# Performance work log

Measured on AMD Instinct MI355X. Metric: run time of the kernel, lower is better.

## Reference

```python
import jax, jax.numpy as jnp
import numpy as np
from jax import lax

B = 4096
PRO_VOCAB, PRO_LEN, PRO_K = 25, 1000, 8
LIG_VOCAB, LIG_LEN, LIG_K = 64, 100, 4
CH = 96  # 2*CH = 192 = 6*32 per the reshape in the original forward
DN = ('NCH', 'OIH', 'NCH')  # 1D conv dimension numbers


def setup_inputs() -> dict:
    key = jax.random.key(0)
    ks = jax.random.split(key, 8)
    protein = jax.random.normal(ks[0], (B, PRO_VOCAB, PRO_LEN), dtype=jnp.float32)
    ligand = jax.random.normal(ks[1], (B, LIG_VOCAB, LIG_LEN), dtype=jnp.float32)
    w_pro = jax.random.normal(ks[2], (CH, PRO_VOCAB, PRO_K), dtype=jnp.float32) * 0.05
    b_pro = jnp.zeros((CH,), dtype=jnp.float32)
    w_lig = jax.random.normal(ks[3], (CH, LIG_VOCAB, LIG_K), dtype=jnp.float32) * 0.05
    b_lig = jnp.zeros((CH,), dtype=jnp.float32)
    # QuLinear readout over the 32*32=1024 amplitude-encoded Gram matrix -> scalar
    w_aff = jax.random.normal(ks[4], (1024,), dtype=jnp.float32) * 0.05
    b_aff = jnp.zeros((), dtype=jnp.float32)
    return {"protein": protein, "ligand": ligand, "w_pro": w_pro, "b_pro": b_pro,
            "w_lig": w_lig, "b_lig": b_lig, "w_aff": w_aff, "b_aff": b_aff}


def _conv_branch(x, w, b):
    # Conv1d (valid) -> ReLU -> global max pool over length  =>  (B, CH)
    y = lax.conv_general_dilated(x, w, (1,), 'VALID', dimension_numbers=DN)
    return jnp.max(jax.nn.relu(y + b[None, :, None]), axis=-1)


def reference(protein, ligand, w_pro, b_pro, w_lig, b_lig, w_aff, b_aff):
    x1 = _conv_branch(ligand, w_lig, b_lig)    # (B, 96)
    x2 = _conv_branch(protein, w_pro, b_pro)   # (B, 96)
    x = jnp.concatenate([x1, x2], axis=1).reshape(-1, 6, 32)  # (B, 6, 32)
    # Vectorized per-sample Gram matrix a.T @ a : (B, 32, 32)
    gram = jnp.einsum('bij,bik->bjk', x, x)
    flat = gram.reshape(gram.shape[0], -1)     # (B, 1024)
    # Amplitude encoding: L2-normalize the flattened Gram matrix per sample
    amp = flat / (jnp.linalg.norm(flat, axis=1, keepdims=True) + 1e-12)
    # QuLinear readout -> scalar affinity per sample
    aff = amp @ w_aff + b_aff                  # (B,)
    return aff
```

## Files before the change

kernel.cpp:

```cpp
#include <hip/hip_runtime.h>
#include <math.h>

typedef _Float16 f16;
typedef _Float16 f16x2 __attribute__((ext_vector_type(2)));
typedef _Float16 f16x4 __attribute__((ext_vector_type(4)));
typedef _Float16 f16x8 __attribute__((ext_vector_type(8)));
typedef float f32x4 __attribute__((ext_vector_type(4)));
typedef float f32x16 __attribute__((ext_vector_type(16)));

template<int V, int K, int VP>
__global__ void repack_kernel(const float* __restrict__ w, f16* __restrict__ wp) {
    int i = blockIdx.x * 256 + threadIdx.x;
    if (i >= K * 96 * VP) return;
    int v = i % VP, ch = (i / VP) % 96, t = i / (VP * 96);
    float val = (v < V) ? w[(ch * V + v) * K + t] : 0.f;
    wp[i] = (f16)val;
}

__global__ void repack_pro_kernel(const float* __restrict__ w, f16* __restrict__ wp) {
    constexpr int V = 25, K = 8;
    int i = blockIdx.x * 256 + threadIdx.x;
    if (i >= K * 6 * 64 * 8) return;
    int e = i & 7, l = (i >> 3) & 63, c6 = (i >> 9) % 6, t = i / (512 * 6);
    int r16 = l & 15, g = l >> 4;
    int ch = c6 * 16 + r16, v = g * 8 + e;
    float val = (v < V) ? w[(ch * V + v) * K + t] : 0.f;
    wp[i] = (f16)val;
}

__global__ __launch_bounds__(256, 2) void conv_pro_kernel(
    const float* __restrict__ in,
    const f16*   __restrict__ wp,
    const float* __restrict__ bias,
    float* __restrict__ feat,
    int feat_off)
{
    constexpr int V = 25, L = 1000, KT = 8, LOUT = 993;
    constexpr int CH  = 256;
    constexpr int NC  = 4;
    constexpr int BR  = 264;
    constexpr int RSB = 80;
    constexpr int P4  = BR / 4;
    constexpr int NVP = 13;
    constexpr int NU  = NVP * P4;
    constexpr int NW  = KT * 6 * 64 * 8;

    __shared__ __align__(16) char s_raw[BR * RSB];
    __shared__ __align__(16) f16  s_w[NW];
    __shared__ float s_red[4 * 96];

    const int tid  = threadIdx.x;
    const int wave = tid >> 6;
    const int lane = tid & 63;
    const int g    = lane >> 4;
    const int r16  = lane & 15;
    const size_t b = blockIdx.x;
    const float* gs = in + b * (size_t)(V * L);

    {
        const f16x8* wg = (const f16x8*)wp;
        f16x8* wl = (f16x8*)s_w;
        #pragma unroll
        for (int u = 0; u < NW / 8 / 256; ++u)
            wl[u * 256 + tid] = wg[u * 256 + tid];
    }
    for (int row = tid; row < BR; row += 256) {
        const int swz = ((row >> 3) & 3) << 4;
        *(f16x8*)(s_raw + row * RSB + (48 ^ swz)) = (f16x8){};
    }
    __syncthreads();

    float runmax[6];
    #pragma unroll
    for (int c6 = 0; c6 < 6; ++c6) runmax[c6] = -3.0e38f;

    for (int c = 0; c < NC; ++c) {
        if (c) __syncthreads();
        #pragma unroll
        for (int u = 0; u < 4; ++u) {
            const int i = u * 256 + tid;
            if (i < NU) {
                const int v2 = i / P4, p4 = i - v2 * P4;
                const int p  = 4 * p4;
                const int gp = c * CH + p;
                float4 x0 = {0.f, 0.f, 0.f, 0.f}, x1 = {0.f, 0.f, 0.f, 0.f};
                if (gp < L) {
                    x0 = *(const float4*)(gs + (size_t)(2 * v2) * L + gp);
                    if (2 * v2 + 1 < V)
                        x1 = *(const float4*)(gs + (size_t)(2 * v2 + 1) * L + gp);
                }
                const int pb = 4 * v2;
                const int slot = pb & 48, sub = pb & 12;
                const float vx0[4] = {x0.x, x0.y, x0.z, x0.w};
                const float vx1[4] = {x1.x, x1.y, x1.z, x1.w};
                #pragma unroll
                for (int j = 0; j < 4; ++j) {
                    const int row = p + j;
                    const int swz = ((row >> 3) & 3) << 4;
                    f16x2 hv = { (f16)vx0[j], (f16)vx1[j] };
                    *(f16x2*)(s_raw + row * RSB + ((slot ^ swz) + sub)) = hv;
                }
            }
        }
        __syncthreads();

        f32x4 acc[4][6] = {};
        #pragma unroll 1
        for (int t = 0; t < KT; ++t) {
            f16x8 bf[6];
            #pragma unroll
            for (int c6 = 0; c6 < 6; ++c6)
                bf[c6] = *(const f16x8*)(s_w + ((t * 6 + c6) * 64 + lane) * 8);
            #pragma unroll
            for (int rt = 0; rt < 4; ++rt) {
                const int row = wave * 64 + rt * 16 + r16 + t;
                const int swz = ((row >> 3) & 3) << 4;
                f16x8 a = *(const f16x8*)(s_raw + row * RSB + ((g * 16) ^ swz));
                #pragma unroll
                for (int c6 = 0; c6 < 6; ++c6)
                    acc[rt][c6] = __builtin_amdgcn_mfma_f32_16x16x32_f16(a, bf[c6], acc[rt][c6], 0, 0, 0);
            }
        }
        #pragma unroll
        for (int rt = 0; rt < 4; ++rt) {
            const int pt = c * CH + wave * 64 + rt * 16;
            if (pt + 16 <= LOUT) {
                #pragma unroll
                for (int c6 = 0; c6 < 6; ++c6)
                    #pragma unroll
                    for (int i = 0; i < 4; ++i)
                        runmax[c6] = fmaxf(runmax[c6], acc[rt][c6][i]);
            } else {
                const int p0g = pt + g * 4;
                #pragma unroll
                for (int c6 = 0; c6 < 6; ++c6)
                    #pragma unroll
                    for (int i = 0; i < 4; ++i)
                        if (p0g + i < LOUT) runmax[c6] = fmaxf(runmax[c6], acc[rt][c6][i]);
            }
        }
    }

    #pragma unroll
    for (int c6 = 0; c6 < 6; ++c6) {
        runmax[c6] = fmaxf(runmax[c6], __shfl_xor(runmax[c6], 16, 64));
        runmax[c6] = fmaxf(runmax[c6], __shfl_xor(runmax[c6], 32, 64));
    }
    if (lane < 16) {
        #pragma unroll
        for (int c6 = 0; c6 < 6; ++c6)
            s_red[wave * 96 + c6 * 16 + lane] = runmax[c6];
    }
    __syncthreads();
    if (tid < 96) {
        float m = fmaxf(fmaxf(s_red[tid], s_red[96 + tid]),
                        fmaxf(s_red[192 + tid], s_red[288 + tid]));
        feat[b * 192 + feat_off + tid] = fmaxf(m + bias[tid], 0.f);
    }
}

__global__ __launch_bounds__(384) void conv_lig_kernel(
    const float* __restrict__ in,
    const f16*   __restrict__ wp,
    const float* __restrict__ bias,
    float* __restrict__ feat,
    int feat_off)
{
    constexpr int V = 64, L = 100, KT = 4, VP = 64, KSTEPS = 4;
    constexpr int LP = 132, RS = 72, NTILES = 4, LOUT = 97;
    constexpr int RSB = RS * 2, NQ = V / 4;
    __shared__ __align__(16) char s_raw[LP * RSB];

    const int tid  = threadIdx.x;
    const int b    = blockIdx.x;
    const int wave = tid >> 6;
    const int lane = tid & 63;
    const int colw = wave % 3;
    const int roww = wave / 3;
    const int q    = lane >> 5;
    const int r    = lane & 31;

    {
        float4 z = {0.f, 0.f, 0.f, 0.f};
        float4* sz = (float4*)s_raw;
        for (int i = tid; i < LP * RSB / 16; i += 384) sz[i] = z;
    }
    __syncthreads();

    const float* gin = in + (size_t)b * (V * L);
    for (int i = tid; i < NQ * L; i += 384) {
        int q4 = i / L, p = i - q4 * L;
        const float* gp = gin + q4 * 4 * L + p;
        f16x4 hv = { (f16)gp[0], (f16)gp[L], (f16)gp[2 * L], (f16)gp[3 * L] };
        int off = (8 * q4) ^ (((p >> 3) & 3) << 4);
        *(f16x4*)(s_raw + p * RSB + off) = hv;
    }

    f16x8 bfr[KT][KSTEPS];
    #pragma unroll
    for (int t = 0; t < KT; ++t)
        #pragma unroll
        for (int ks = 0; ks < KSTEPS; ++ks)
            bfr[t][ks] = *(const f16x8*)(wp + (t * 96 + colw * 32 + r) * VP + ks * 16 + q * 8);

    __syncthreads();

    float runmax = -3.0e38f;
    for (int it = 0; it < NTILES / 2; ++it) {
        const int p0 = (roww * (NTILES / 2) + it) * 32;
        f32x16 acc = {};
        #pragma unroll
        for (int t = 0; t < KT; ++t) {
            int row = p0 + r + t;
            if (row > LP - 1) row = LP - 1;
            const char* ap = s_raw + row * RSB;
            const int swz = ((row >> 3) & 3) << 4;
            #pragma unroll
            for (int ks = 0; ks < KSTEPS; ++ks) {
                f16x8 af = *(const f16x8*)(ap + ((ks * 32 + q * 16) ^ swz));
                acc = __builtin_amdgcn_mfma_f32_32x32x16_f16(af, bfr[t][ks], acc, 0, 0, 0);
            }
        }
        #pragma unroll
        for (int i = 0; i < 16; ++i) {
            int rr = (i & 3) + 8 * (i >> 2) + 4 * q;
            if (p0 + rr < LOUT) runmax = fmaxf(runmax, acc[i]);
        }
    }
    runmax = fmaxf(runmax, __shfl_xor(runmax, 32, 64));

    __syncthreads();
    float* s_red = (float*)s_raw;
    if (lane < 32) s_red[roww * 96 + colw * 32 + r] = runmax;
    __syncthreads();
    if (tid < 96) {
        float m = fmaxf(s_red[tid], s_red[96 + tid]);
        feat[(size_t)b * 192 + feat_off + tid] = fmaxf(m + bias[tid], 0.f);
    }
}

__global__ __launch_bounds__(256) void gram_affinity_kernel(
    const float* __restrict__ feat, const float* __restrict__ w_aff,
    const float* __restrict__ b_aff, float* __restrict__ out, int B)
{
    const int lane = threadIdx.x & 63;
    const int wid  = threadIdx.x >> 6;
    const int b    = blockIdx.x * 4 + wid;

    __shared__ float s_x[4][192];

    if (b < B) {
        const float* fp = feat + (size_t)b * 192;
        for (int i = lane; i < 192; i += 64) s_x[wid][i] = fp[i];
    }
    __syncthreads();

    if (b < B) {
        float ssum = 0.f, sdot = 0.f;
        #pragma unroll
        for (int t = 0; t < 16; ++t) {
            const int jk = t * 64 + lane;
            const int j = jk >> 5, k = jk & 31;
            float gg = 0.f;
            #pragma unroll
            for (int i = 0; i < 6; ++i)
                gg = fmaf(s_x[wid][i * 32 + j], s_x[wid][i * 32 + k], gg);
            ssum = fmaf(gg, gg, ssum);
            sdot = fmaf(gg, w_aff[jk], sdot);
        }
        #pragma unroll
        for (int off = 32; off >= 1; off >>= 1) {
            ssum += __shfl_xor(ssum, off, 64);
            sdot += __shfl_xor(sdot, off, 64);
        }
        if (lane == 0) out[b] = sdot / (sqrtf(ssum) + 1e-12f) + b_aff[0];
    }
}

extern "C" void kernel_launch(void* const* d_in, const int* in_sizes, int n_in,
                              void* d_out, int out_size, void* d_ws, size_t ws_size,
                              hipStream_t stream)
{
    const float* protein = (const float*)d_in[0];
    const float* ligand  = (const float*)d_in[1];
    const float* w_pro   = (const float*)d_in[2];
    const float* b_pro   = (const float*)d_in[3];
    const float* w_lig   = (const float*)d_in[4];
    const float* b_lig   = (const float*)d_in[5];
    const float* w_aff   = (const float*)d_in[6];
    const float* b_aff   = (const float*)d_in[7];
    float* out = (float*)d_out;
    const int B = out_size;

    float* feat   = (float*)d_ws;
    f16*   wpackP = (f16*)((char*)d_ws + (size_t)B * 192 * 4);
    f16*   wpackL = wpackP + 24576;

    repack_pro_kernel<<<96, 256, 0, stream>>>(w_pro, wpackP);
    repack_kernel<64, 4, 64><<<96, 256, 0, stream>>>(w_lig, wpackL);

    conv_lig_kernel<<<B, 384, 0, stream>>>(ligand, wpackL, b_lig, feat, 0);
    conv_pro_kernel<<<B, 256, 0, stream>>>(protein, wpackP, b_pro, feat, 96);

    gram_affinity_kernel<<<(B + 3) / 4, 256, 0, stream>>>(feat, w_aff, b_aff, out, B);
}
```

Before: 301.0 us.

## Double-buffer protein conv input chunks with register prefetch and smaller chunks

Splits the protein sequence into 8 chunks of 128 positions instead of 4 chunks of 256, and adds two LDS buffers. The global loads for the next chunk are issued into registers before the MFMA loop and written to the other buffer afterwards. This lets global memory latency overlap with the MFMA compute. In exchange each chunk does half as many MFMA row tiles per wave, adds more barriers, and keeps prefetched values live in registers.

```diff
diff --git a/kernel.cpp b/kernel.cpp
--- a/kernel.cpp
+++ b/kernel.cpp
@@ -36,16 +36,16 @@
     int feat_off)
 {
     constexpr int V = 25, L = 1000, KT = 8, LOUT = 993;
-    constexpr int CH  = 256;
-    constexpr int NC  = 4;
-    constexpr int BR  = 264;
+    constexpr int CH  = 128;
+    constexpr int NC  = 8;
+    constexpr int BR  = 136;
     constexpr int RSB = 80;
     constexpr int P4  = BR / 4;
     constexpr int NVP = 13;
     constexpr int NU  = NVP * P4;
     constexpr int NW  = KT * 6 * 64 * 8;
 
-    __shared__ __align__(16) char s_raw[BR * RSB];
+    __shared__ __align__(16) char s_buf[2][BR * RSB];
     __shared__ __align__(16) f16  s_w[NW];
     __shared__ float s_red[4 * 96];
 
@@ -57,54 +57,93 @@
     const size_t b = blockIdx.x;
     const float* gs = in + b * (size_t)(V * L);
 
-    {
-        const f16x8* wg = (const f16x8*)wp;
-        f16x8* wl = (f16x8*)s_w;
-        #pragma unroll
-        for (int u = 0; u < NW / 8 / 256; ++u)
-            wl[u * 256 + tid] = wg[u * 256 + tid];
-    }
-    for (int row = tid; row < BR; row += 256) {
-        const int swz = ((row >> 3) & 3) << 4;
-        *(f16x8*)(s_raw + row * RSB + (48 ^ swz)) = (f16x8){};
-    }
-    __syncthreads();
-
-    float runmax[6];
-    #pragma unroll
-    for (int c6 = 0; c6 < 6; ++c6) runmax[c6] = -3.0e38f;
-
-    for (int c = 0; c < NC; ++c) {
-        if (c) __syncthreads();
-        #pragma unroll
-        for (int u = 0; u < 4; ++u) {
-            const int i = u * 256 + tid;
+    float4 xa0, xa1, xb0, xb1;
+
+    auto issue_loads = [&](int c) {
+        const float4 z4 = {0.f, 0.f, 0.f, 0.f};
+        {
+            const int v2 = tid / P4, p4 = tid - v2 * P4;
+            const int gp = c * CH + 4 * p4;
+            xa0 = z4; xa1 = z4;
+            if (gp < L) {
+                xa0 = *(const float4*)(gs + (size_t)(2 * v2) * L + gp);
+                xa1 = *(const float4*)(gs + (size_t)(2 * v2 + 1) * L + gp);
+            }
+        }
+        {
+            const int i = 256 + tid;
+            xb0 = z4; xb1 = z4;
             if (i < NU) {
                 const int v2 = i / P4, p4 = i - v2 * P4;
-                const int p  = 4 * p4;
-                const int gp = c * CH + p;
-                float4 x0 = {0.f, 0.f, 0.f, 0.f}, x1 = {0.f, 0.f, 0.f, 0.f};
+                const int gp = c * CH + 4 * p4;
                 if (gp < L) {
-                    x0 = *(const float4*)(gs + (size_t)(2 * v2) * L + gp);
+                    xb0 = *(const float4*)(gs + (size_t)(2 * v2) * L + gp);
                     if (2 * v2 + 1 < V)
-                        x1 = *(const float4*)(gs + (size_t)(2 * v2 + 1) * L + gp);
+                        xb1 = *(const float4*)(gs + (size_t)(2 * v2 + 1) * L + gp);
                 }
-                const int pb = 4 * v2;
+            }
+        }
+    };
+
+    auto write_rs = [&](char* sb) {
+        {   const int v2 = tid / P4, p4 = tid - v2 * P4;
+            const int p = 4 * p4, pb = 4 * v2;
+            const int slot = pb & 48, sub = pb & 12;
+            const float va[4] = {xa0.x, xa0.y, xa0.z, xa0.w};
+            const float vb[4] = {xa1.x, xa1.y, xa1.z, xa1.w};
+            #pragma unroll
+            for (int j = 0; j < 4; ++j) {
+                const int row = p + j;
+                const int swz = ((row >> 3) & 3) << 4;
+                f16x2 hv = { (f16)va[j], (f16)vb[j] };
+                *(f16x2*)(sb + row * RSB + ((slot ^ swz) + sub)) = hv;
+            }
+        }
+        {   const int i = 256 + tid;
+            if (i < NU) {
+                const int v2 = i / P4, p4 = i - v2 * P4;
+                const int p = 4 * p4, pb = 4 * v2;
                 const int slot = pb & 48, sub = pb & 12;
-                const float vx0[4] = {x0.x, x0.y, x0.z, x0.w};
-                const float vx1[4] = {x1.x, x1.y, x1.z, x1.w};
+                const float va[4] = {xb0.x, xb0.y, xb0.z, xb0.w};
+                const float vb[4] = {xb1.x, xb1.y, xb1.z, xb1.w};
                 #pragma unroll
                 for (int j = 0; j < 4; ++j) {
                     const int row = p + j;
                     const int swz = ((row >> 3) & 3) << 4;
-                    f16x2 hv = { (f16)vx0[j], (f16)vx1[j] };
-                    *(f16x2*)(s_raw + row * RSB + ((slot ^ swz) + sub)) = hv;
+                    f16x2 hv = { (f16)va[j], (f16)vb[j] };
+                    *(f16x2*)(sb + row * RSB + ((slot ^ swz) + sub)) = hv;
                 }
             }
         }
-        __syncthreads();
-
-        f32x4 acc[4][6] = {};
+    };
+
+    issue_loads(0);
+    {
+        const f16x8* wg = (const f16x8*)wp;
+        f16x8* wl = (f16x8*)s_w;
+        #pragma unroll
+        for (int u = 0; u < NW / 8 / 256; ++u)
+            wl[u * 256 + tid] = wg[u * 256 + tid];
+    }
+    for (int i = tid; i < 2 * BR; i += 256) {
+        const int bsel = i / BR, row = i - bsel * BR;
+        const int swz = ((row >> 3) & 3) << 4;
+        *(f16x8*)(&s_buf[bsel][0] + row * RSB + (48 ^ swz)) = (f16x8){};
+    }
+    __syncthreads();
+    write_rs(&s_buf[0][0]);
+    __syncthreads();
+
+    float runmax[6];
+    #pragma unroll
+    for (int c6 = 0; c6 < 6; ++c6) runmax[c6] = -3.0e38f;
+
+    for (int c = 0; c < NC; ++c) {
+        if (c + 1 < NC) issue_loads(c + 1);
+        __builtin_amdgcn_sched_barrier(0);
+
+        const char* sb = &s_buf[c & 1][0];
+        f32x4 acc[2][6] = {};
         #pragma unroll 1
         for (int t = 0; t < KT; ++t) {
             f16x8 bf[6];
@@ -112,18 +151,18 @@
             for (int c6 = 0; c6 < 6; ++c6)
                 bf[c6] = *(const f16x8*)(s_w + ((t * 6 + c6) * 64 + lane) * 8);
             #pragma unroll
-            for (int rt = 0; rt < 4; ++rt) {
-                const int row = wave * 64 + rt * 16 + r16 + t;
+            for (int rt = 0; rt < 2; ++rt) {
+                const int row = wave * 32 + rt * 16 + r16 + t;
                 const int swz = ((row >> 3) & 3) << 4;
-                f16x8 a = *(const f16x8*)(s_raw + row * RSB + ((g * 16) ^ swz));
+                f16x8 a = *(const f16x8*)(sb + row * RSB + ((g * 16) ^ swz));
                 #pragma unroll
                 for (int c6 = 0; c6 < 6; ++c6)
                     acc[rt][c6] = __builtin_amdgcn_mfma_f32_16x16x32_f16(a, bf[c6], acc[rt][c6], 0, 0, 0);
             }
         }
         #pragma unroll
-        for (int rt = 0; rt < 4; ++rt) {
-            const int pt = c * CH + wave * 64 + rt * 16;
+        for (int rt = 0; rt < 2; ++rt) {
+            const int pt = c * CH + wave * 32 + rt * 16;
             if (pt + 16 <= LOUT) {
                 #pragma unroll
                 for (int c6 = 0; c6 < 6; ++c6)
@@ -139,6 +178,9 @@
                         if (p0g + i < LOUT) runmax[c6] = fmaxf(runmax[c6], acc[rt][c6][i]);
             }
         }
+
+        if (c + 1 < NC) write_rs(&s_buf[(c + 1) & 1][0]);
+        __syncthreads();
     }
 
     #pragma unroll
```

New measurement: 290.6 us. 3.5% less time.
